# Optimization experiments

Hardware: AMD Instinct MI355X
Metric: run time of the kernel (lower is better)

Reference implementation:

```python
import jax, jax.numpy as jnp
import numpy as np

B, S, D, H, K, V = 4, 2048, 768, 12, 64, 64

def setup_inputs() -> dict:
    key = jax.random.key(0)
    ks = jax.random.split(key, 8)
    return {
        "queries": jax.random.normal(ks[0], (B, S, D), dtype=jnp.float32),
        "keys": jax.random.normal(ks[1], (B, S, D), dtype=jnp.float32),
        "values": jax.random.normal(ks[2], (B, S, D), dtype=jnp.float32),
        "mask": jnp.ones((1, 1, S, S), dtype=jnp.float32),
        "W_q": jax.random.normal(ks[3], (H, D, K), dtype=jnp.float32) * 0.02,
        "W_k": jax.random.normal(ks[4], (H, D, K), dtype=jnp.float32) * 0.02,
        "W_v": jax.random.normal(ks[5], (H, D, V), dtype=jnp.float32) * 0.02,
        "W_o": jax.random.normal(ks[6], (H * V, D), dtype=jnp.float32) * 0.02,
    }

def reference(queries, keys, values, mask, W_q, W_k, W_v, W_o):
    # per-head projections: np.dot([B,S,D],[H,D,K]) -> [B,S,H,K] -> transpose -> [B,H,S,K]
    q = jnp.einsum('bsd,hdk->bhsk', queries, W_q)
    k = jnp.einsum('bsd,hdk->bhsk', keys, W_k)
    v = jnp.einsum('bsd,hdv->bhsv', values, W_v)
    scale = 1.0 / jnp.sqrt(jnp.float32(K))
    logits = jnp.einsum('bhqk,bhmk->bhqm', q, k) * scale  # [B,H,S,S]
    logits = logits + (1.0 - mask) * (-1e9)
    attn = jax.nn.softmax(logits, axis=-1)
    o = jnp.einsum('bhqm,bhmv->bhqv', attn, v)  # [B,H,S,V]
    # original does a RAW reshape [B,H,S,V] -> [B,S,H*V] (no transpose) -- faithful
    o = o.reshape(B, S, H * V)
    return jnp.einsum('bsf,fd->bsd', o, W_o)
```

## Files before the change

kernel.cpp:

```cpp
#include <hip/hip_runtime.h>
#include <hip/hip_bf16.h>


typedef __attribute__((ext_vector_type(8))) short short8;
typedef __attribute__((ext_vector_type(4))) short s16x4;
typedef __attribute__((ext_vector_type(4))) float f32x4;
typedef __attribute__((ext_vector_type(16))) float f32x16;
typedef __attribute__((ext_vector_type(2))) int int2v;
typedef __attribute__((ext_vector_type(4))) int int4v;

#define NB 4
#define NS 2048
#define ND 768
#define NH 12
#define HD 64

#define QSCALE 0.18033688011112043f
#define NLOG2E (-1.4426950408889634e9f)

__device__ __forceinline__ unsigned short f2bf(float f){
    __hip_bfloat16 h = __float2bfloat16(f);
    return __builtin_bit_cast(unsigned short, h);
}

#define OFF_BIAS ((size_t)0)
#define OFF_FLAG ((size_t)33554432)
#define OFF_WQ  ((size_t)37748736)
#define OFF_WK  ((size_t)38928384)
#define OFF_WV  ((size_t)40108032)
#define OFF_WO  ((size_t)41287680)
#define OFF_Q   ((size_t)42467328)
#define OFF_K   ((size_t)55050240)
#define OFF_V   ((size_t)67633152)
#define OFF_O   ((size_t)80216064)

__global__ __launch_bounds__(256) void bias_kernel(
    const float* __restrict__ mask, float* __restrict__ biasf,
    unsigned* __restrict__ flag){
    size_t t = (size_t)blockIdx.x*256 + threadIdx.x;
    f32x4 a = reinterpret_cast<const f32x4*>(mask)[2*t];
    f32x4 b = reinterpret_cast<const f32x4*>(mask)[2*t+1];
    f32x4 oa, ob;
    bool nz = false;
    for(int i=0;i<4;i++){
        oa[i] = (1.0f-a[i])*NLOG2E; ob[i] = (1.0f-b[i])*NLOG2E;
        nz = nz || (oa[i] != 0.0f) || (ob[i] != 0.0f);
    }
    reinterpret_cast<f32x4*>(biasf)[2*t]   = oa;
    reinterpret_cast<f32x4*>(biasf)[2*t+1] = ob;
    if(nz) atomicOr(flag, 1u);
}

__global__ __launch_bounds__(256) void packw_kernel(
    const float* __restrict__ Wq, const float* __restrict__ Wk,
    const float* __restrict__ Wv, const float* __restrict__ Wo,
    unsigned short* __restrict__ wq, unsigned short* __restrict__ wk,
    unsigned short* __restrict__ wv, unsigned short* __restrict__ wo,
    unsigned* __restrict__ flag){
    if(blockIdx.x==0 && blockIdx.y==0 && threadIdx.x==0) *flag = 0u;
    int y = blockIdx.y, x = blockIdx.x;
    const float* src; unsigned short* dst; int sstr, r0, c0;
    if(y < 3){
        const float* W = y==0 ? Wq : (y==1 ? Wk : Wv);
        unsigned short* o = y==0 ? wq : (y==1 ? wk : wv);
        int h = x/12, dt = x%12;
        src = W + (size_t)h*ND*HD; sstr = HD; r0 = dt*64; c0 = 0;
        dst = o + (size_t)h*HD*ND;
    } else {
        src = Wo; sstr = ND; r0 = (x/12)*64; c0 = (x%12)*64;
        dst = wo;
    }
    __shared__ unsigned short T[64*68];
    int t = threadIdx.x;
    int tr = t>>4, tc4 = (t&15)*4;
    for(int it=0; it<4; it++){
        int r = it*16 + tr;
        f32x4 vv = *reinterpret_cast<const f32x4*>(src + (size_t)(r0+r)*sstr + c0 + tc4);
        s16x4 p; p[0]=(short)f2bf(vv[0]); p[1]=(short)f2bf(vv[1]);
                 p[2]=(short)f2bf(vv[2]); p[3]=(short)f2bf(vv[3]);
        *reinterpret_cast<s16x4*>(&T[r*68 + tc4]) = p;
    }
    __syncthreads();
    for(int it=0; it<4; it++){
        int c = it*16 + tr;
        s16x4 p;
        p[0] = (short)T[(tc4+0)*68 + c];
        p[1] = (short)T[(tc4+1)*68 + c];
        p[2] = (short)T[(tc4+2)*68 + c];
        p[3] = (short)T[(tc4+3)*68 + c];
        *reinterpret_cast<s16x4*>(dst + (size_t)(c0+c)*ND + r0 + tc4) = p;
    }
}

#define LDP 72
#define CPT 136
__global__ __launch_bounds__(256) void gemm_proj(
    const float* __restrict__ qf, const float* __restrict__ kf,
    const unsigned short* __restrict__ wq, const unsigned short* __restrict__ wk,
    unsigned short* __restrict__ oq, unsigned short* __restrict__ ok){
    int z = blockIdx.z;
    const float* Af          = z==0 ? qf : kf;
    const unsigned short* Bt = z==0 ? wq : wk;
    unsigned short* dst      = z==0 ? oq : ok;
    const float qsc          = z==0 ? QSCALE : 1.0f;

    __shared__ alignas(16) unsigned short smem[2*128*LDP];
    unsigned short* As = smem;
    unsigned short* Bs = smem + 128*LDP;
    int tid = threadIdx.x;
    int lane = tid & 63, wave = tid >> 6;
    int l15 = lane & 15, quad = lane >> 4;
    int wm = (wave >> 1)*64, wn = (wave & 1)*64;
    int tm = blockIdx.x*128, tn = blockIdx.y*128;

    f32x4 acc[4][4] = {};
    for(int k0 = 0; k0 < ND; k0 += 64){
        __syncthreads();
        for(int i = 0; i < 4; i++){
            int flat = i*256 + tid;
            int row = flat >> 3, cb = flat & 7;
            f32x4 a0 = *reinterpret_cast<const f32x4*>(Af + (size_t)(tm+row)*ND + k0 + cb*8);
            f32x4 a1 = *reinterpret_cast<const f32x4*>(Af + (size_t)(tm+row)*ND + k0 + cb*8 + 4);
            short8 av;
            av[0]=(short)f2bf(a0[0]); av[1]=(short)f2bf(a0[1]); av[2]=(short)f2bf(a0[2]); av[3]=(short)f2bf(a0[3]);
            av[4]=(short)f2bf(a1[0]); av[5]=(short)f2bf(a1[1]); av[6]=(short)f2bf(a1[2]); av[7]=(short)f2bf(a1[3]);
            *reinterpret_cast<short8*>(&As[row*LDP + cb*8]) = av;
            *reinterpret_cast<short8*>(&Bs[row*LDP + cb*8]) =
                *reinterpret_cast<const short8*>(Bt + (size_t)(tn+row)*ND + k0 + cb*8);
        }
        __syncthreads();
        for(int ks = 0; ks < 2; ks++){
            short8 af[4], bf[4];
            for(int i = 0; i < 4; i++)
                af[i] = *reinterpret_cast<const short8*>(&As[(wm + i*16 + l15)*LDP + ks*32 + quad*8]);
            for(int j = 0; j < 4; j++)
                bf[j] = *reinterpret_cast<const short8*>(&Bs[(wn + j*16 + l15)*LDP + ks*32 + quad*8]);
            for(int i = 0; i < 4; i++)
                for(int j = 0; j < 4; j++)
                    acc[i][j] = __builtin_amdgcn_mfma_f32_16x16x32_bf16(af[i], bf[j], acc[i][j], 0, 0, 0);
        }
    }
    __syncthreads();
    unsigned short* Cs = smem;
    for(int i = 0; i < 4; i++)
        for(int j = 0; j < 4; j++)
            for(int r = 0; r < 4; r++)
                Cs[(wm + i*16 + quad*4 + r)*CPT + wn + j*16 + l15] = f2bf(acc[i][j][r]*qsc);
    __syncthreads();
    for(int c8 = 0; c8 < 8; c8++){
        int idx = c8*256 + tid;
        int row = idx >> 4, ch = idx & 15;
        short8 val = *reinterpret_cast<const short8*>(&Cs[row*CPT + ch*8]);
        int m = tm + row, n = tn + ch*8;
        int b = m >> 11, s = m & 2047, h = n >> 6, kk = n & 63;
        *reinterpret_cast<short8*>(dst + ((size_t)(b*NH + h)*NS + s)*HD + kk) = val;
    }
}

__global__ __launch_bounds__(256) void gemm_projT(
    const unsigned short* __restrict__ A,
    const float* __restrict__ Bf,
    unsigned short* __restrict__ dst){
    __shared__ alignas(16) unsigned short smem[2*128*LDP];
    unsigned short* As = smem;
    unsigned short* Bs = smem + 128*LDP;
    int tid = threadIdx.x;
    int lane = tid & 63, wave = tid >> 6;
    int l15 = lane & 15, quad = lane >> 4;
    int wm = (wave >> 1)*64, wn = (wave & 1)*64;
    int tm = blockIdx.x*128, tn = blockIdx.y*128;

    f32x4 acc[4][4] = {};
    for(int k0 = 0; k0 < ND; k0 += 64){
        __syncthreads();
        for(int i = 0; i < 4; i++){
            int flat = i*256 + tid;
            int row = flat >> 3, cb = flat & 7;
            *reinterpret_cast<short8*>(&As[row*LDP + cb*8]) =
                *reinterpret_cast<const short8*>(A + (size_t)(tm+row)*ND + k0 + cb*8);
            f32x4 b0 = *reinterpret_cast<const f32x4*>(Bf + (size_t)(tn+row)*ND + k0 + cb*8);
            f32x4 b1 = *reinterpret_cast<const f32x4*>(Bf + (size_t)(tn+row)*ND + k0 + cb*8 + 4);
            short8 bv;
            bv[0]=(short)f2bf(b0[0]); bv[1]=(short)f2bf(b0[1]); bv[2]=(short)f2bf(b0[2]); bv[3]=(short)f2bf(b0[3]);
            bv[4]=(short)f2bf(b1[0]); bv[5]=(short)f2bf(b1[1]); bv[6]=(short)f2bf(b1[2]); bv[7]=(short)f2bf(b1[3]);
            *reinterpret_cast<short8*>(&Bs[row*LDP + cb*8]) = bv;
        }
        __syncthreads();
        for(int ks = 0; ks < 2; ks++){
            short8 af[4], bf[4];
            for(int i = 0; i < 4; i++)
                af[i] = *reinterpret_cast<const short8*>(&As[(wm + i*16 + l15)*LDP + ks*32 + quad*8]);
            for(int j = 0; j < 4; j++)
                bf[j] = *reinterpret_cast<const short8*>(&Bs[(wn + j*16 + l15)*LDP + ks*32 + quad*8]);
            for(int i = 0; i < 4; i++)
                for(int j = 0; j < 4; j++)
                    acc[i][j] = __builtin_amdgcn_mfma_f32_16x16x32_bf16(af[i], bf[j], acc[i][j], 0, 0, 0);
        }
    }
    __syncthreads();
    unsigned short* Cs = smem;
    for(int i = 0; i < 4; i++)
        for(int j = 0; j < 4; j++)
            for(int r = 0; r < 4; r++)
                Cs[(wm + i*16 + quad*4 + r)*CPT + wn + j*16 + l15] = f2bf(acc[i][j][r]);
    __syncthreads();
    int b = tn >> 11, s0 = tn & 2047;
    for(int c8 = 0; c8 < 8; c8++){
        int idx = c8*256 + tid;
        int row = idx >> 4, ch = idx & 15;
        short8 val = *reinterpret_cast<const short8*>(&Cs[row*CPT + ch*8]);
        int h = (tm + row) >> 6, kk = (tm + row) & 63;
        *reinterpret_cast<short8*>(dst + ((size_t)(b*NH + h)*HD + kk)*NS + s0 + ch*8) = val;
    }
}

__global__ __launch_bounds__(256, 3) void attn3_kernel(
    const unsigned short* __restrict__ qws, const unsigned short* __restrict__ kws,
    const unsigned short* __restrict__ vtws, const float* __restrict__ biasf,
    const unsigned* __restrict__ bflag, unsigned short* __restrict__ ows){
    const int bh = blockIdx.y, qt = blockIdx.x;
    const int tid = threadIdx.x, lane = tid & 63, wave = tid >> 6;
    const int l31 = lane & 31, hi = lane >> 5;

    __shared__ alignas(16) unsigned short Ks[2][64*72];
    __shared__ alignas(16) unsigned short Vs[3][64*72];

    const size_t bhq = (size_t)bh * NS;
    const int qb0 = qt*128 + wave*32;
    const bool hasBias = (*bflag != 0u);

    short8 bq[4];
    #pragma unroll
    for(int ds=0; ds<4; ds++)
        bq[ds] = *reinterpret_cast<const short8*>(
            qws + (bhq + qb0 + l31)*HD + ds*16 + hi*8);

    const float* bp = biasf + (size_t)(qb0 + l31)*NS + hi*4;

    const int rS = tid >> 3;
    const int cS = tid & 7;

    short8 rk[2], rv[2];
    #define LOADK(i,KT) rk[i] = *reinterpret_cast<const short8*>(kws + (bhq + (size_t)(KT)*64 + (i)*32 + rS)*HD + cS*8)
    #define LOADV(i,KT) rv[i] = *reinterpret_cast<const short8*>(vtws + ((size_t)bh*HD + (i)*32 + rS)*NS + (size_t)(KT)*64 + cS*8)

    #define STAGE(KB, VB)                                                         \
    {                                                                             \
        _Pragma("unroll")                                                         \
        for(int i=0;i<2;i++){                                                     \
            int row = i*32 + rS;                                                  \
            *reinterpret_cast<short8*>(&Ks[KB][row*72 + cS*8]) = rk[i];           \
            *reinterpret_cast<short8*>(&Vs[VB][row*72 + cS*8]) = rv[i];           \
        }                                                                         \
    }

    #define QK(KB)                                                                \
    {                                                                             \
        _Pragma("unroll")                                                         \
        for(int kb=0; kb<2; kb++){                                                \
            f32x16 zt = {};                                                       \
            _Pragma("unroll")                                                     \
            for(int ds=0; ds<4; ds++){                                            \
                short8 ak = *reinterpret_cast<const short8*>(                     \
                    &Ks[KB][(kb*32 + l31)*72 + ds*16 + hi*8]);                    \
                zt = __builtin_amdgcn_mfma_f32_32x32x16_bf16(ak, bq[ds], zt, 0, 0, 0);\
            }                                                                     \
            z2[kb] = zt;                                                          \
        }                                                                         \
    }

    #define SMAX(KT)                                                              \
    {                                                                             \
        _Pragma("unroll")                                                         \
        for(int kb=0; kb<2; kb++){                                                \
            f32x4 bb[4];                                                          \
            if(hasBias){                                                          \
                _Pragma("unroll")                                                 \
                for(int g=0; g<4; g++)                                            \
                    bb[g] = *reinterpret_cast<const f32x4*>(bp + (KT)*64 + kb*32 + g*8);\
            } else {                                                              \
                _Pragma("unroll")                                                 \
                for(int g=0; g<4; g++){ bb[g][0]=0.f; bb[g][1]=0.f; bb[g][2]=0.f; bb[g][3]=0.f; } \
            }                                                                     \
            unsigned p[8];                                                        \
            _Pragma("unroll")                                                     \
            for(int g=0; g<4; g++){                                               \
                float e0 = exp2f(z2[kb][g*4+0] + bb[g][0]);                       \
                float e1 = exp2f(z2[kb][g*4+1] + bb[g][1]);                       \
                float e2 = exp2f(z2[kb][g*4+2] + bb[g][2]);                       \
                float e3 = exp2f(z2[kb][g*4+3] + bb[g][3]);                       \
                p[g*2+0] = (unsigned)f2bf(e0) | ((unsigned)f2bf(e1) << 16);       \
                p[g*2+1] = (unsigned)f2bf(e2) | ((unsigned)f2bf(e3) << 16);       \
            }                                                                     \
            int2v sA = __builtin_amdgcn_permlane32_swap((int)p[0], (int)p[2], false, false); \
            int2v sB = __builtin_amdgcn_permlane32_swap((int)p[1], (int)p[3], false, false); \
            int2v sC = __builtin_amdgcn_permlane32_swap((int)p[4], (int)p[6], false, false); \
            int2v sD = __builtin_amdgcn_permlane32_swap((int)p[5], (int)p[7], false, false); \
            int4v f0; f0[0]=sA[0]; f0[1]=sB[0]; f0[2]=sA[1]; f0[3]=sB[1];         \
            int4v f1; f1[0]=sC[0]; f1[1]=sD[0]; f1[2]=sC[1]; f1[3]=sD[1];         \
            afragP[kb*2+0] = __builtin_bit_cast(short8, f0);                      \
            afragP[kb*2+1] = __builtin_bit_cast(short8, f1);                      \
        }                                                                         \
    }

    #define PVACC(VB)                                                             \
    {                                                                             \
        _Pragma("unroll")                                                         \
        for(int kst=0; kst<4; kst++){                                             \
            zacc = __builtin_amdgcn_mfma_f32_32x32x16_bf16(afragP[kst], vone, zacc, 0, 0, 0); \
            _Pragma("unroll")                                                     \
            for(int nb=0; nb<2; nb++){                                            \
                short8 bv = *reinterpret_cast<const short8*>(                     \
                    &Vs[VB][(nb*32 + l31)*72 + kst*16 + hi*8]);                   \
                oacc[nb] = __builtin_amdgcn_mfma_f32_32x32x16_bf16(afragP[kst], bv, oacc[nb], 0, 0, 0); \
            }                                                                     \
        }                                                                         \
    }

    f32x16 oacc[2] = {};
    f32x16 zacc = {};
    f32x16 z2[2];
    short8 afragP[4];
    short8 vone;
    #pragma unroll
    for(int i=0;i<8;i++) vone[i] = (short)0x3F80;

    LOADK(0,0); LOADK(1,0); LOADV(0,0); LOADV(1,0);
    STAGE(0, 0)
    __syncthreads();
    LOADK(0,1); LOADK(1,1); LOADV(0,1); LOADV(1,1);
    __builtin_amdgcn_s_setprio(1);
    QK(0)
    __builtin_amdgcn_s_setprio(0);
    SMAX(0)

    for(int kt = 1; kt < 32; kt++){
        const int cb = kt & 1;
        const int vb = kt % 3;
        const int vp = (kt-1) % 3;
        STAGE(cb, vb)
        __syncthreads();
        int ktn = kt < 31 ? kt+1 : 31;
        LOADK(0,ktn); LOADK(1,ktn); LOADV(0,ktn); LOADV(1,ktn);

        __builtin_amdgcn_s_setprio(1);
        QK(cb)
        PVACC(vp)
        __builtin_amdgcn_s_setprio(0);
        SMAX(kt)
    }
    {
        const int vp = 31 % 3;
        __builtin_amdgcn_s_setprio(1);
        PVACC(vp)
        __builtin_amdgcn_s_setprio(0);
    }

    float inv[16];
    #pragma unroll
    for(int r=0;r<16;r++) inv[r] = 1.0f / zacc[r];
    #pragma unroll
    for(int nb=0;nb<2;nb++)
        #pragma unroll
        for(int r=0;r<16;r++){
            int q = qb0 + (r&3) + 8*(r>>2) + 4*hi;
            ows[(bhq + q)*HD + nb*32 + l31] = f2bf(oacc[nb][r]*inv[r]);
        }
    #undef LOADK
    #undef LOADV
    #undef STAGE
    #undef QK
    #undef SMAX
    #undef PVACC
}

__global__ __launch_bounds__(256) void gemm_out(
    const unsigned short* __restrict__ A, const unsigned short* __restrict__ Bt,
    float* __restrict__ out){
    __shared__ alignas(16) unsigned short As[128*LDP];
    __shared__ alignas(16) unsigned short Bs[128*LDP];
    int tid = threadIdx.x;
    int lane = tid & 63, wave = tid >> 6;
    int l15 = lane & 15, quad = lane >> 4;
    int wm = (wave >> 1)*64, wn = (wave & 1)*64;
    int tm = blockIdx.x*128, tn = blockIdx.y*128;

    f32x4 acc[4][4] = {};
    for(int k0 = 0; k0 < ND; k0 += 64){
        __syncthreads();
        for(int i = 0; i < 4; i++){
            int flat = i*256 + tid;
            int row = flat >> 3, cb = flat & 7;
            *reinterpret_cast<short8*>(&As[row*LDP + cb*8]) =
                *reinterpret_cast<const short8*>(A  + (size_t)(tm+row)*ND + k0 + cb*8);
            *reinterpret_cast<short8*>(&Bs[row*LDP + cb*8]) =
                *reinterpret_cast<const short8*>(Bt + (size_t)(tn+row)*ND + k0 + cb*8);
        }
        __syncthreads();
        for(int ks = 0; ks < 2; ks++){
            short8 af[4], bf[4];
            for(int i = 0; i < 4; i++)
                af[i] = *reinterpret_cast<const short8*>(&As[(wm + i*16 + l15)*LDP + ks*32 + quad*8]);
            for(int j = 0; j < 4; j++)
                bf[j] = *reinterpret_cast<const short8*>(&Bs[(wn + j*16 + l15)*LDP + ks*32 + quad*8]);
            for(int i = 0; i < 4; i++)
                for(int j = 0; j < 4; j++)
                    acc[i][j] = __builtin_amdgcn_mfma_f32_16x16x32_bf16(af[i], bf[j], acc[i][j], 0, 0, 0);
        }
    }
    for(int i = 0; i < 4; i++)
        for(int j = 0; j < 4; j++)
            for(int r = 0; r < 4; r++){
                int m = tm + wm + i*16 + quad*4 + r;
                int n = tn + wn + j*16 + l15;
                out[(size_t)m*ND + n] = acc[i][j][r];
            }
}

extern "C" void kernel_launch(void* const* d_in, const int* in_sizes, int n_in,
                              void* d_out, int out_size, void* d_ws, size_t ws_size,
                              hipStream_t stream){
    const float* q    = (const float*)d_in[0];
    const float* k    = (const float*)d_in[1];
    const float* v    = (const float*)d_in[2];
    const float* mask = (const float*)d_in[3];
    const float* Wq   = (const float*)d_in[4];
    const float* Wk   = (const float*)d_in[5];
    const float* Wv   = (const float*)d_in[6];
    const float* Wo   = (const float*)d_in[7];
    char* ws = (char*)d_ws;
    float*          biasf = (float*)(ws + OFF_BIAS);
    unsigned*       bflag = (unsigned*)(ws + OFF_FLAG);
    unsigned short* wqp= (unsigned short*)(ws + OFF_WQ);
    unsigned short* wkp= (unsigned short*)(ws + OFF_WK);
    unsigned short* wvp= (unsigned short*)(ws + OFF_WV);
    unsigned short* wop= (unsigned short*)(ws + OFF_WO);
    unsigned short* qw = (unsigned short*)(ws + OFF_Q);
    unsigned short* kw = (unsigned short*)(ws + OFF_K);
    unsigned short* vw = (unsigned short*)(ws + OFF_V);
    unsigned short* ow = (unsigned short*)(ws + OFF_O);

    packw_kernel<<<dim3(144, 4), 256, 0, stream>>>(Wq, Wk, Wv, Wo, wqp, wkp, wvp, wop, bflag);
    bias_kernel<<<dim3(2048), 256, 0, stream>>>(mask, biasf, bflag);
    gemm_proj<<<dim3(64, 6, 2), 256, 0, stream>>>(q, k, wqp, wkp, qw, kw);
    gemm_projT<<<dim3(6, 64), 256, 0, stream>>>(wvp, v, vw);
    attn3_kernel<<<dim3(16, 48), 256, 0, stream>>>(qw, kw, vw, biasf, bflag, ow);
    gemm_out<<<dim3(64, 6), 256, 0, stream>>>(ow, wop, (float*)d_out);
}
```

Before: 311.9 us.

## Pre-cast activations to bf16 and stage GEMM tiles with direct global-to-LDS loads

Adds a cast kernel that converts q, k and v to bf16 once, into workspace regions and the output buffer reused as scratch. The three projection and output GEMMs then load tiles with global_load_lds straight into unpadded LDS instead of going through registers and converting in-loop. This removes the conversion ALU work and register staging from the GEMM loops, at the cost of an extra full pass over the fp32 inputs. The unpadded 64-element row stride may also cause LDS bank conflicts on the MFMA fragment reads.

```diff
diff --git a/kernel.cpp b/kernel.cpp
--- a/kernel.cpp
+++ b/kernel.cpp
@@ -23,7 +23,14 @@
     return __builtin_bit_cast(unsigned short, h);
 }
 
+__device__ __forceinline__ void gload16(const void* g, void* l){
+    __builtin_amdgcn_global_load_lds(
+        (const __attribute__((address_space(1))) void*)g,
+        (__attribute__((address_space(3))) void*)l, 16, 0, 0);
+}
+
 #define OFF_BIAS ((size_t)0)
+#define OFF_QB  ((size_t)16777216)
 #define OFF_FLAG ((size_t)33554432)
 #define OFF_WQ  ((size_t)37748736)
 #define OFF_WK  ((size_t)38928384)
@@ -49,6 +56,22 @@
     reinterpret_cast<f32x4*>(biasf)[2*t]   = oa;
     reinterpret_cast<f32x4*>(biasf)[2*t+1] = ob;
     if(nz) atomicOr(flag, 1u);
+}
+
+__global__ __launch_bounds__(256) void cast_kernel(
+    const float* __restrict__ q, const float* __restrict__ k,
+    const float* __restrict__ v, unsigned short* __restrict__ qb,
+    unsigned short* __restrict__ kb, unsigned short* __restrict__ vb){
+    int y = blockIdx.y;
+    const float* src = y==0 ? q : (y==1 ? k : v);
+    unsigned short* dst = y==0 ? qb : (y==1 ? kb : vb);
+    size_t t = (size_t)blockIdx.x*256 + threadIdx.x;
+    f32x4 a = reinterpret_cast<const f32x4*>(src)[2*t];
+    f32x4 b = reinterpret_cast<const f32x4*>(src)[2*t+1];
+    short8 o;
+    o[0]=(short)f2bf(a[0]); o[1]=(short)f2bf(a[1]); o[2]=(short)f2bf(a[2]); o[3]=(short)f2bf(a[3]);
+    o[4]=(short)f2bf(b[0]); o[5]=(short)f2bf(b[1]); o[6]=(short)f2bf(b[2]); o[7]=(short)f2bf(b[3]);
+    reinterpret_cast<short8*>(dst)[t] = o;
 }
 
 __global__ __launch_bounds__(256) void packw_kernel(
@@ -92,21 +115,20 @@
     }
 }
 
-#define LDP 72
 #define CPT 136
 __global__ __launch_bounds__(256) void gemm_proj(
-    const float* __restrict__ qf, const float* __restrict__ kf,
+    const unsigned short* __restrict__ qb, const unsigned short* __restrict__ kb,
     const unsigned short* __restrict__ wq, const unsigned short* __restrict__ wk,
     unsigned short* __restrict__ oq, unsigned short* __restrict__ ok){
     int z = blockIdx.z;
-    const float* Af          = z==0 ? qf : kf;
+    const unsigned short* Af = z==0 ? qb : kb;
     const unsigned short* Bt = z==0 ? wq : wk;
     unsigned short* dst      = z==0 ? oq : ok;
     const float qsc          = z==0 ? QSCALE : 1.0f;
 
-    __shared__ alignas(16) unsigned short smem[2*128*LDP];
+    __shared__ alignas(16) unsigned short smem[128*CPT];
     unsigned short* As = smem;
-    unsigned short* Bs = smem + 128*LDP;
+    unsigned short* Bs = smem + 128*64;
     int tid = threadIdx.x;
     int lane = tid & 63, wave = tid >> 6;
     int l15 = lane & 15, quad = lane >> 4;
@@ -116,25 +138,20 @@
     f32x4 acc[4][4] = {};
     for(int k0 = 0; k0 < ND; k0 += 64){
         __syncthreads();
-        for(int i = 0; i < 4; i++){
-            int flat = i*256 + tid;
-            int row = flat >> 3, cb = flat & 7;
-            f32x4 a0 = *reinterpret_cast<const f32x4*>(Af + (size_t)(tm+row)*ND + k0 + cb*8);
-            f32x4 a1 = *reinterpret_cast<const f32x4*>(Af + (size_t)(tm+row)*ND + k0 + cb*8 + 4);
-            short8 av;
-            av[0]=(short)f2bf(a0[0]); av[1]=(short)f2bf(a0[1]); av[2]=(short)f2bf(a0[2]); av[3]=(short)f2bf(a0[3]);
-            av[4]=(short)f2bf(a1[0]); av[5]=(short)f2bf(a1[1]); av[6]=(short)f2bf(a1[2]); av[7]=(short)f2bf(a1[3]);
-            *reinterpret_cast<short8*>(&As[row*LDP + cb*8]) = av;
-            *reinterpret_cast<short8*>(&Bs[row*LDP + cb*8]) =
-                *reinterpret_cast<const short8*>(Bt + (size_t)(tn+row)*ND + k0 + cb*8);
+        const unsigned short* ga = Af + (size_t)(tm + wave*32 + (lane>>3))*ND + k0 + (lane&7)*8;
+        const unsigned short* gb = Bt + (size_t)(tn + wave*32 + (lane>>3))*ND + k0 + (lane&7)*8;
+        #pragma unroll
+        for(int it=0; it<4; it++){
+            gload16(ga + (size_t)(it*8)*ND, &As[(wave*32+it*8)*64]);
+            gload16(gb + (size_t)(it*8)*ND, &Bs[(wave*32+it*8)*64]);
         }
         __syncthreads();
         for(int ks = 0; ks < 2; ks++){
             short8 af[4], bf[4];
             for(int i = 0; i < 4; i++)
-                af[i] = *reinterpret_cast<const short8*>(&As[(wm + i*16 + l15)*LDP + ks*32 + quad*8]);
+                af[i] = *reinterpret_cast<const short8*>(&As[(wm + i*16 + l15)*64 + ks*32 + quad*8]);
             for(int j = 0; j < 4; j++)
-                bf[j] = *reinterpret_cast<const short8*>(&Bs[(wn + j*16 + l15)*LDP + ks*32 + quad*8]);
+                bf[j] = *reinterpret_cast<const short8*>(&Bs[(wn + j*16 + l15)*64 + ks*32 + quad*8]);
             for(int i = 0; i < 4; i++)
                 for(int j = 0; j < 4; j++)
                     acc[i][j] = __builtin_amdgcn_mfma_f32_16x16x32_bf16(af[i], bf[j], acc[i][j], 0, 0, 0);
@@ -159,11 +176,11 @@
 
 __global__ __launch_bounds__(256) void gemm_projT(
     const unsigned short* __restrict__ A,
-    const float* __restrict__ Bf,
+    const unsigned short* __restrict__ Bv,
     unsigned short* __restrict__ dst){
-    __shared__ alignas(16) unsigned short smem[2*128*LDP];
+    __shared__ alignas(16) unsigned short smem[128*CPT];
     unsigned short* As = smem;
-    unsigned short* Bs = smem + 128*LDP;
+    unsigned short* Bs = smem + 128*64;
     int tid = threadIdx.x;
     int lane = tid & 63, wave = tid >> 6;
     int l15 = lane & 15, quad = lane >> 4;
@@ -173,25 +190,20 @@
     f32x4 acc[4][4] = {};
     for(int k0 = 0; k0 < ND; k0 += 64){
         __syncthreads();
-        for(int i = 0; i < 4; i++){
-            int flat = i*256 + tid;
-            int row = flat >> 3, cb = flat & 7;
-            *reinterpret_cast<short8*>(&As[row*LDP + cb*8]) =
-                *reinterpret_cast<const short8*>(A + (size_t)(tm+row)*ND + k0 + cb*8);
-            f32x4 b0 = *reinterpret_cast<const f32x4*>(Bf + (size_t)(tn+row)*ND + k0 + cb*8);
-            f32x4 b1 = *reinterpret_cast<const f32x4*>(Bf + (size_t)(tn+row)*ND + k0 + cb*8 + 4);
-            short8 bv;
-            bv[0]=(short)f2bf(b0[0]); bv[1]=(short)f2bf(b0[1]); bv[2]=(short)f2bf(b0[2]); bv[3]=(short)f2bf(b0[3]);
-            bv[4]=(short)f2bf(b1[0]); bv[5]=(short)f2bf(b1[1]); bv[6]=(short)f2bf(b1[2]); bv[7]=(short)f2bf(b1[3]);
-            *reinterpret_cast<short8*>(&Bs[row*LDP + cb*8]) = bv;
+        const unsigned short* ga = A  + (size_t)(tm + wave*32 + (lane>>3))*ND + k0 + (lane&7)*8;
+        const unsigned short* gb = Bv + (size_t)(tn + wave*32 + (lane>>3))*ND + k0 + (lane&7)*8;
+        #pragma unroll
+        for(int it=0; it<4; it++){
+            gload16(ga + (size_t)(it*8)*ND, &As[(wave*32+it*8)*64]);
+            gload16(gb + (size_t)(it*8)*ND, &Bs[(wave*32+it*8)*64]);
         }
         __syncthreads();
         for(int ks = 0; ks < 2; ks++){
             short8 af[4], bf[4];
             for(int i = 0; i < 4; i++)
-                af[i] = *reinterpret_cast<const short8*>(&As[(wm + i*16 + l15)*LDP + ks*32 + quad*8]);
+                af[i] = *reinterpret_cast<const short8*>(&As[(wm + i*16 + l15)*64 + ks*32 + quad*8]);
             for(int j = 0; j < 4; j++)
-                bf[j] = *reinterpret_cast<const short8*>(&Bs[(wn + j*16 + l15)*LDP + ks*32 + quad*8]);
+                bf[j] = *reinterpret_cast<const short8*>(&Bs[(wn + j*16 + l15)*64 + ks*32 + quad*8]);
             for(int i = 0; i < 4; i++)
                 for(int j = 0; j < 4; j++)
                     acc[i][j] = __builtin_amdgcn_mfma_f32_16x16x32_bf16(af[i], bf[j], acc[i][j], 0, 0, 0);
@@ -377,8 +389,9 @@
 __global__ __launch_bounds__(256) void gemm_out(
     const unsigned short* __restrict__ A, const unsigned short* __restrict__ Bt,
     float* __restrict__ out){
-    __shared__ alignas(16) unsigned short As[128*LDP];
-    __shared__ alignas(16) unsigned short Bs[128*LDP];
+    __shared__ alignas(16) unsigned short smem[2*128*64];
+    unsigned short* As = smem;
+    unsigned short* Bs = smem + 128*64;
     int tid = threadIdx.x;
     int lane = tid & 63, wave = tid >> 6;
     int l15 = lane & 15, quad = lane >> 4;
@@ -388,21 +401,20 @@
     f32x4 acc[4][4] = {};
     for(int k0 = 0; k0 < ND; k0 += 64){
         __syncthreads();
-        for(int i = 0; i < 4; i++){
-            int flat = i*256 + tid;
-            int row = flat >> 3, cb = flat & 7;
-            *reinterpret_cast<short8*>(&As[row*LDP + cb*8]) =
-                *reinterpret_cast<const short8*>(A  + (size_t)(tm+row)*ND + k0 + cb*8);
-            *reinterpret_cast<short8*>(&Bs[row*LDP + cb*8]) =
-                *reinterpret_cast<const short8*>(Bt + (size_t)(tn+row)*ND + k0 + cb*8);
+        const unsigned short* ga = A  + (size_t)(tm + wave*32 + (lane>>3))*ND + k0 + (lane&7)*8;
+        const unsigned short* gb = Bt + (size_t)(tn + wave*32 + (lane>>3))*ND + k0 + (lane&7)*8;
+        #pragma unroll
+        for(int it=0; it<4; it++){
+            gload16(ga + (size_t)(it*8)*ND, &As[(wave*32+it*8)*64]);
+            gload16(gb + (size_t)(it*8)*ND, &Bs[(wave*32+it*8)*64]);
         }
         __syncthreads();
         for(int ks = 0; ks < 2; ks++){
             short8 af[4], bf[4];
             for(int i = 0; i < 4; i++)
-                af[i] = *reinterpret_cast<const short8*>(&As[(wm + i*16 + l15)*LDP + ks*32 + quad*8]);
+                af[i] = *reinterpret_cast<const short8*>(&As[(wm + i*16 + l15)*64 + ks*32 + quad*8]);
             for(int j = 0; j < 4; j++)
-                bf[j] = *reinterpret_cast<const short8*>(&Bs[(wn + j*16 + l15)*LDP + ks*32 + quad*8]);
+                bf[j] = *reinterpret_cast<const short8*>(&Bs[(wn + j*16 + l15)*64 + ks*32 + quad*8]);
             for(int i = 0; i < 4; i++)
                 for(int j = 0; j < 4; j++)
                     acc[i][j] = __builtin_amdgcn_mfma_f32_16x16x32_bf16(af[i], bf[j], acc[i][j], 0, 0, 0);
@@ -439,11 +451,15 @@
     unsigned short* kw = (unsigned short*)(ws + OFF_K);
     unsigned short* vw = (unsigned short*)(ws + OFF_V);
     unsigned short* ow = (unsigned short*)(ws + OFF_O);
+    unsigned short* qb = (unsigned short*)(ws + OFF_QB);
+    unsigned short* kb = (unsigned short*)(ws + OFF_O);
+    unsigned short* vb = (unsigned short*)d_out;
 
     packw_kernel<<<dim3(144, 4), 256, 0, stream>>>(Wq, Wk, Wv, Wo, wqp, wkp, wvp, wop, bflag);
     bias_kernel<<<dim3(2048), 256, 0, stream>>>(mask, biasf, bflag);
-    gemm_proj<<<dim3(64, 6, 2), 256, 0, stream>>>(q, k, wqp, wkp, qw, kw);
-    gemm_projT<<<dim3(6, 64), 256, 0, stream>>>(wvp, v, vw);
+    cast_kernel<<<dim3(3072, 3), 256, 0, stream>>>(q, k, v, qb, kb, vb);
+    gemm_proj<<<dim3(64, 6, 2), 256, 0, stream>>>(qb, kb, wqp, wkp, qw, kw);
+    gemm_projT<<<dim3(6, 64), 256, 0, stream>>>(wvp, vb, vw);
     attn3_kernel<<<dim3(16, 48), 256, 0, stream>>>(qw, kw, vw, biasf, bflag, ow);
     gemm_out<<<dim3(64, 6), 256, 0, stream>>>(ow, wop, (float*)d_out);
 }
```

New measurement: 325.3 us. 4.3% more time.
